# Performance work log

Measured on AMD Instinct MI355X. Metric: run time of the kernel, lower is better.

## Reference

```python
import jax, jax.numpy as jnp
import numpy as np

D_MODEL = 1024
GEOM_DIM = 32
CLAMP_VALUE = 10.0


def setup_inputs() -> dict:
    key = jax.random.key(0)
    k1, k2, k3 = jax.random.split(key, 3)
    B, N = 4, 2048
    H = jax.random.normal(k1, (B, N, D_MODEL), dtype=jnp.float32)
    B_prev = jax.random.normal(k2, (B, N, N), dtype=jnp.float32)
    # geom_proj weight, init std=0.001 as in the torch module
    W = jax.random.normal(k3, (GEOM_DIM, D_MODEL), dtype=jnp.float32) * 0.001
    alpha = jnp.asarray(1.0, dtype=jnp.float32)
    beta = jnp.asarray(0.05, dtype=jnp.float32)
    return {"H": H, "B_prev": B_prev, "W": W, "alpha": alpha, "beta": beta}


def reference(H, B_prev, W, alpha, beta):
    # Low-rank projection: G [B, N, geom_dim]
    G = jnp.einsum("bnd,kd->bnk", H, W)
    G_sq = jnp.sum(G * G, axis=-1)  # [B, N]
    # Pairwise squared distance: [B, N, N]
    gram = jnp.einsum("bik,bjk->bij", G, G)
    dist = G_sq[:, :, None] + G_sq[:, None, :] - 2.0 * gram
    dist = jnp.maximum(dist, 0.0)
    # EMA bias update with clamp
    B_next = alpha * B_prev - beta * dist
    B_next = jnp.clip(B_next, -CLAMP_VALUE, CLAMP_VALUE)
    return B_next
```

## Files before the change

### kernel.cpp

```cpp
#include <hip/hip_runtime.h>


typedef __attribute__((ext_vector_type(8))) short short8;
typedef __attribute__((ext_vector_type(4))) float floatx4;

static __device__ __forceinline__ short bf16_bits(float f) {
    union { float f; unsigned int u; } v; v.f = f;
    unsigned int u = v.u;
    u += 0x7FFFu + ((u >> 16) & 1u);
    return (short)(u >> 16);
}

__global__ __launch_bounds__(256) void k1_proj(const float* __restrict__ H,
                                               const float* __restrict__ W,
                                               float* __restrict__ G,
                                               float* __restrict__ Q) {
    const int blk  = blockIdx.x;
    const int t    = threadIdx.x;
    const int w    = t >> 6;
    const int lane = t & 63;
    const int m    = lane & 15;
    const int quad = lane >> 4;

    const float* hrow  = H + ((long)blk * 16 + m) * 1024;
    const float* wrow0 = W + (long)m * 1024;
    const float* wrow1 = W + (long)(m + 16) * 1024;

    const int kq = w * 256 + quad * 8;

    floatx4 acc0 = {0.f, 0.f, 0.f, 0.f};
    floatx4 acc1 = {0.f, 0.f, 0.f, 0.f};

    float4 a0  = *(const float4*)(hrow  + kq);
    float4 a1  = *(const float4*)(hrow  + kq + 4);
    float4 b00 = *(const float4*)(wrow0 + kq);
    float4 b01 = *(const float4*)(wrow0 + kq + 4);
    float4 b10 = *(const float4*)(wrow1 + kq);
    float4 b11 = *(const float4*)(wrow1 + kq + 4);

    #pragma unroll
    for (int step = 0; step < 8; ++step) {
        float4 na0, na1, nb00, nb01, nb10, nb11;
        if (step < 7) {
            const int nk = kq + (step + 1) * 32;
            na0  = *(const float4*)(hrow  + nk);
            na1  = *(const float4*)(hrow  + nk + 4);
            nb00 = *(const float4*)(wrow0 + nk);
            nb01 = *(const float4*)(wrow0 + nk + 4);
            nb10 = *(const float4*)(wrow1 + nk);
            nb11 = *(const float4*)(wrow1 + nk + 4);
        }
        short8 af, bf0, bf1;
        af[0] = bf16_bits(a0.x);  af[1] = bf16_bits(a0.y);
        af[2] = bf16_bits(a0.z);  af[3] = bf16_bits(a0.w);
        af[4] = bf16_bits(a1.x);  af[5] = bf16_bits(a1.y);
        af[6] = bf16_bits(a1.z);  af[7] = bf16_bits(a1.w);
        bf0[0] = bf16_bits(b00.x); bf0[1] = bf16_bits(b00.y);
        bf0[2] = bf16_bits(b00.z); bf0[3] = bf16_bits(b00.w);
        bf0[4] = bf16_bits(b01.x); bf0[5] = bf16_bits(b01.y);
        bf0[6] = bf16_bits(b01.z); bf0[7] = bf16_bits(b01.w);
        bf1[0] = bf16_bits(b10.x); bf1[1] = bf16_bits(b10.y);
        bf1[2] = bf16_bits(b10.z); bf1[3] = bf16_bits(b10.w);
        bf1[4] = bf16_bits(b11.x); bf1[5] = bf16_bits(b11.y);
        bf1[6] = bf16_bits(b11.z); bf1[7] = bf16_bits(b11.w);

        acc0 = __builtin_amdgcn_mfma_f32_16x16x32_bf16(af, bf0, acc0, 0, 0, 0);
        acc1 = __builtin_amdgcn_mfma_f32_16x16x32_bf16(af, bf1, acc1, 0, 0, 0);

        if (step < 7) { a0 = na0; a1 = na1; b00 = nb00; b01 = nb01; b10 = nb10; b11 = nb11; }
    }

    __shared__ float red[4][16][32];
    #pragma unroll
    for (int r = 0; r < 4; ++r) {
        red[w][quad * 4 + r][m]      = acc0[r];
        red[w][quad * 4 + r][m + 16] = acc1[r];
    }
    __syncthreads();
    for (int e = t; e < 512; e += 256) {
        const int mm = e >> 5, nn = e & 31;
        float v = red[0][mm][nn] + red[1][mm][nn] + red[2][mm][nn] + red[3][mm][nn];
        G[(long)(blk * 16 + mm) * 32 + nn] = v;
        red[0][mm][nn] = v;
    }
    __syncthreads();
    if (t < 16) {
        float s = 0.f;
        #pragma unroll
        for (int nn = 0; nn < 32; ++nn) { const float v = red[0][t][nn]; s += v * v; }
        Q[blk * 16 + t] = s;
    }
}

__global__ __launch_bounds__(256) void k2_update(const float* __restrict__ Bp,
                                                 const float* __restrict__ G,
                                                 const float* __restrict__ Q,
                                                 const float* __restrict__ alphap,
                                                 const float* __restrict__ betap,
                                                 float* __restrict__ out) {
    __shared__ float4 sGi[128 * 8];
    __shared__ float4 sGj[128 * 8];
    __shared__ float  sQi[128];
    __shared__ float  sQj[128];

    const int b  = blockIdx.z;
    const int i0 = blockIdx.y * 128;
    const int j0 = blockIdx.x * 128;
    const int t  = threadIdx.x;

    const float4* Gi4 = (const float4*)(G + ((long)b * 2048 + i0) * 32);
    const float4* Gj4 = (const float4*)(G + ((long)b * 2048 + j0) * 32);
    #pragma unroll
    for (int l = 0; l < 4; ++l) {
        const int f = t + l * 256;
        const int r = f >> 3, c = f & 7;
        const int cs = c ^ ((r >> 3) & 7);
        sGi[r * 8 + cs] = Gi4[f];
        sGj[r * 8 + cs] = Gj4[f];
    }
    if (t < 128) sQi[t] = Q[b * 2048 + i0 + t];
    else         sQj[t - 128] = Q[b * 2048 + j0 + (t - 128)];
    __syncthreads();

    const int tx = t & 15;
    const int ty = t >> 4;

    float acc[8][8];
    #pragma unroll
    for (int ii = 0; ii < 8; ++ii)
        #pragma unroll
        for (int jj = 0; jj < 8; ++jj) acc[ii][jj] = 0.f;

    #pragma unroll
    for (int c = 0; c < 8; ++c) {
        float4 gi[8], gj[8];
        #pragma unroll
        for (int u = 0; u < 8; ++u) {
            const int ri = ty * 8 + u;
            gi[u] = sGi[ri * 8 + (c ^ ((ri >> 3) & 7))];
            const int rj = tx * 8 + u;
            gj[u] = sGj[rj * 8 + (c ^ ((rj >> 3) & 7))];
        }
        #pragma unroll
        for (int ii = 0; ii < 8; ++ii)
            #pragma unroll
            for (int jj = 0; jj < 8; ++jj)
                acc[ii][jj] += gi[ii].x * gj[jj].x + gi[ii].y * gj[jj].y +
                               gi[ii].z * gj[jj].z + gi[ii].w * gj[jj].w;
    }

    const float alpha = alphap[0];
    const float beta  = betap[0];

    #pragma unroll
    for (int ii = 0; ii < 8; ++ii) {
        const int i = i0 + ty * 8 + ii;
        const long rowoff = ((long)b * 2048 + i) * 2048 + j0;
        const float4* bp = (const float4*)(Bp + rowoff);
        float4*       op = (float4*)(out + rowoff);
        const float qi = sQi[ty * 8 + ii];
        #pragma unroll
        for (int g = 0; g < 2; ++g) {
            const float4 bv = bp[tx * 2 + g];
            float4 ov;
            {
                const int jj = g * 4 + 0;
                float d = qi + sQj[tx * 8 + jj] - 2.f * acc[ii][jj];
                d = fmaxf(d, 0.f);
                ov.x = fminf(fmaxf(alpha * bv.x - beta * d, -10.f), 10.f);
            }
            {
                const int jj = g * 4 + 1;
                float d = qi + sQj[tx * 8 + jj] - 2.f * acc[ii][jj];
                d = fmaxf(d, 0.f);
                ov.y = fminf(fmaxf(alpha * bv.y - beta * d, -10.f), 10.f);
            }
            {
                const int jj = g * 4 + 2;
                float d = qi + sQj[tx * 8 + jj] - 2.f * acc[ii][jj];
                d = fmaxf(d, 0.f);
                ov.z = fminf(fmaxf(alpha * bv.z - beta * d, -10.f), 10.f);
            }
            {
                const int jj = g * 4 + 3;
                float d = qi + sQj[tx * 8 + jj] - 2.f * acc[ii][jj];
                d = fmaxf(d, 0.f);
                ov.w = fminf(fmaxf(alpha * bv.w - beta * d, -10.f), 10.f);
            }
            op[tx * 2 + g] = ov;
        }
    }
}

extern "C" void kernel_launch(void* const* d_in, const int* in_sizes, int n_in,
                              void* d_out, int out_size, void* d_ws, size_t ws_size,
                              hipStream_t stream) {
    const float* H     = (const float*)d_in[0];
    const float* Bp    = (const float*)d_in[1];
    const float* W     = (const float*)d_in[2];
    const float* alpha = (const float*)d_in[3];
    const float* beta  = (const float*)d_in[4];
    float* out = (float*)d_out;

    float* G = (float*)d_ws;
    float* Q = G + 8192 * 32;

    k1_proj<<<512, 256, 0, stream>>>(H, W, G, Q);

    dim3 g2(16, 16, 4);
    k2_update<<<g2, 256, 0, stream>>>(Bp, G, Q, alpha, beta, out);
}
```

Measured before the change: 168.5 us.

## Compute gram matrix with bf16 MFMA and store projection as bf16

The projection kernel now stores G as bf16 and computes the squared norms from the rounded values. The update kernel replaces the scalar fp32 FMA gram computation with 16x16x32 bf16 MFMA instructions and halves the i-tile to 64 rows, which doubles the grid. It also drops the XOR-swizzled shared layout in favour of a padded one. The output store pattern changes from float4 per thread to scalar strided stores across lanes, which may reduce store vectorisation, and bf16 G adds precision loss to the distance.

```diff
diff --git a/kernel.cpp b/kernel.cpp
--- a/kernel.cpp
+++ b/kernel.cpp
@@ -11,9 +11,14 @@
     return (short)(u >> 16);
 }
 
+static __device__ __forceinline__ float bf16_to_f32(unsigned short h) {
+    union { unsigned int u; float f; } v; v.u = ((unsigned int)h) << 16;
+    return v.f;
+}
+
 __global__ __launch_bounds__(256) void k1_proj(const float* __restrict__ H,
                                                const float* __restrict__ W,
-                                               float* __restrict__ G,
+                                               unsigned short* __restrict__ G,
                                                float* __restrict__ Q) {
     const int blk  = blockIdx.x;
     const int t    = threadIdx.x;
@@ -80,8 +85,9 @@
     for (int e = t; e < 512; e += 256) {
         const int mm = e >> 5, nn = e & 31;
         float v = red[0][mm][nn] + red[1][mm][nn] + red[2][mm][nn] + red[3][mm][nn];
-        G[(long)(blk * 16 + mm) * 32 + nn] = v;
-        red[0][mm][nn] = v;
+        const unsigned short hb = (unsigned short)bf16_bits(v);
+        G[(long)(blk * 16 + mm) * 32 + nn] = hb;
+        red[0][mm][nn] = bf16_to_f32(hb);
     }
     __syncthreads();
     if (t < 16) {
@@ -93,101 +99,74 @@
 }
 
 __global__ __launch_bounds__(256) void k2_update(const float* __restrict__ Bp,
-                                                 const float* __restrict__ G,
+                                                 const unsigned short* __restrict__ G,
                                                  const float* __restrict__ Q,
                                                  const float* __restrict__ alphap,
                                                  const float* __restrict__ betap,
                                                  float* __restrict__ out) {
-    __shared__ float4 sGi[128 * 8];
-    __shared__ float4 sGj[128 * 8];
-    __shared__ float  sQi[128];
-    __shared__ float  sQj[128];
+    __shared__ short sGi[64 * 40];
+    __shared__ short sGj[128 * 40];
+    __shared__ float sQi[64];
+    __shared__ float sQj[128];
 
     const int b  = blockIdx.z;
-    const int i0 = blockIdx.y * 128;
+    const int i0 = blockIdx.y * 64;
     const int j0 = blockIdx.x * 128;
     const int t  = threadIdx.x;
 
-    const float4* Gi4 = (const float4*)(G + ((long)b * 2048 + i0) * 32);
-    const float4* Gj4 = (const float4*)(G + ((long)b * 2048 + j0) * 32);
+    const short* Gg = (const short*)G;
+    {
+        const int r = t >> 2, c = t & 3;
+        *(short8*)&sGi[r * 40 + c * 8] =
+            *(const short8*)&Gg[(long)(b * 2048 + i0 + r) * 32 + c * 8];
+    }
     #pragma unroll
-    for (int l = 0; l < 4; ++l) {
+    for (int l = 0; l < 2; ++l) {
         const int f = t + l * 256;
-        const int r = f >> 3, c = f & 7;
-        const int cs = c ^ ((r >> 3) & 7);
-        sGi[r * 8 + cs] = Gi4[f];
-        sGj[r * 8 + cs] = Gj4[f];
+        const int r = f >> 2, c = f & 3;
+        *(short8*)&sGj[r * 40 + c * 8] =
+            *(const short8*)&Gg[(long)(b * 2048 + j0 + r) * 32 + c * 8];
     }
-    if (t < 128) sQi[t] = Q[b * 2048 + i0 + t];
-    else         sQj[t - 128] = Q[b * 2048 + j0 + (t - 128)];
+    if (t < 64)       sQi[t]      = Q[b * 2048 + i0 + t];
+    else if (t < 192) sQj[t - 64] = Q[b * 2048 + j0 + (t - 64)];
     __syncthreads();
 
-    const int tx = t & 15;
-    const int ty = t >> 4;
+    const int w    = t >> 6;
+    const int lane = t & 63;
+    const int m    = lane & 15;
+    const int quad = lane >> 4;
 
-    float acc[8][8];
+    const short8 af = *(const short8*)&sGi[(w * 16 + m) * 40 + quad * 8];
+    floatx4 acc[8];
     #pragma unroll
-    for (int ii = 0; ii < 8; ++ii)
-        #pragma unroll
-        for (int jj = 0; jj < 8; ++jj) acc[ii][jj] = 0.f;
-
-    #pragma unroll
-    for (int c = 0; c < 8; ++c) {
-        float4 gi[8], gj[8];
-        #pragma unroll
-        for (int u = 0; u < 8; ++u) {
-            const int ri = ty * 8 + u;
-            gi[u] = sGi[ri * 8 + (c ^ ((ri >> 3) & 7))];
-            const int rj = tx * 8 + u;
-            gj[u] = sGj[rj * 8 + (c ^ ((rj >> 3) & 7))];
-        }
-        #pragma unroll
-        for (int ii = 0; ii < 8; ++ii)
-            #pragma unroll
-            for (int jj = 0; jj < 8; ++jj)
-                acc[ii][jj] += gi[ii].x * gj[jj].x + gi[ii].y * gj[jj].y +
-                               gi[ii].z * gj[jj].z + gi[ii].w * gj[jj].w;
+    for (int jt = 0; jt < 8; ++jt) {
+        const short8 bf = *(const short8*)&sGj[(jt * 16 + m) * 40 + quad * 8];
+        floatx4 z = {0.f, 0.f, 0.f, 0.f};
+        acc[jt] = __builtin_amdgcn_mfma_f32_16x16x32_bf16(af, bf, z, 0, 0, 0);
     }
 
     const float alpha = alphap[0];
     const float beta  = betap[0];
 
+    float qj[8];
     #pragma unroll
-    for (int ii = 0; ii < 8; ++ii) {
-        const int i = i0 + ty * 8 + ii;
-        const long rowoff = ((long)b * 2048 + i) * 2048 + j0;
-        const float4* bp = (const float4*)(Bp + rowoff);
-        float4*       op = (float4*)(out + rowoff);
-        const float qi = sQi[ty * 8 + ii];
+    for (int jt = 0; jt < 8; ++jt) qj[jt] = sQj[jt * 16 + m];
+
+    const long base = (long)b * 2048 * 2048;
+    #pragma unroll
+    for (int r = 0; r < 4; ++r) {
+        const int i = i0 + w * 16 + quad * 4 + r;
+        const float qi = sQi[w * 16 + quad * 4 + r];
+        const float* bprow = Bp  + base + (long)i * 2048 + j0 + m;
+        float*       orow  = out + base + (long)i * 2048 + j0 + m;
+        float bv[8];
         #pragma unroll
-        for (int g = 0; g < 2; ++g) {
-            const float4 bv = bp[tx * 2 + g];
-            float4 ov;
-            {
-                const int jj = g * 4 + 0;
-                float d = qi + sQj[tx * 8 + jj] - 2.f * acc[ii][jj];
-                d = fmaxf(d, 0.f);
-                ov.x = fminf(fmaxf(alpha * bv.x - beta * d, -10.f), 10.f);
-            }
-            {
-                const int jj = g * 4 + 1;
-                float d = qi + sQj[tx * 8 + jj] - 2.f * acc[ii][jj];
-                d = fmaxf(d, 0.f);
-                ov.y = fminf(fmaxf(alpha * bv.y - beta * d, -10.f), 10.f);
-            }
-            {
-                const int jj = g * 4 + 2;
-                float d = qi + sQj[tx * 8 + jj] - 2.f * acc[ii][jj];
-                d = fmaxf(d, 0.f);
-                ov.z = fminf(fmaxf(alpha * bv.z - beta * d, -10.f), 10.f);
-            }
-            {
-                const int jj = g * 4 + 3;
-                float d = qi + sQj[tx * 8 + jj] - 2.f * acc[ii][jj];
-                d = fmaxf(d, 0.f);
-                ov.w = fminf(fmaxf(alpha * bv.w - beta * d, -10.f), 10.f);
-            }
-            op[tx * 2 + g] = ov;
+        for (int jt = 0; jt < 8; ++jt) bv[jt] = bprow[jt * 16];
+        #pragma unroll
+        for (int jt = 0; jt < 8; ++jt) {
+            float d = qi + qj[jt] - 2.f * acc[jt][r];
+            d = fmaxf(d, 0.f);
+            orow[jt * 16] = fminf(fmaxf(alpha * bv[jt] - beta * d, -10.f), 10.f);
         }
     }
 }
@@ -202,11 +181,11 @@
     const float* beta  = (const float*)d_in[4];
     float* out = (float*)d_out;
 
-    float* G = (float*)d_ws;
-    float* Q = G + 8192 * 32;
+    unsigned short* G = (unsigned short*)d_ws;
+    float* Q = (float*)((char*)d_ws + 8192 * 32 * 2);
 
     k1_proj<<<512, 256, 0, stream>>>(H, W, G, Q);
 
-    dim3 g2(16, 16, 4);
+    dim3 g2(16, 32, 4);
     k2_update<<<g2, 256, 0, stream>>>(Bp, G, Q, alpha, beta, out);
 }
```

Result: faster. 158.2 us (-6.1%).
